# Optimization experiments

Hardware: AMD Instinct MI355X
Metric: run time of the kernel (lower is better)

The kernel has to match this reference:

```python
import jax, jax.numpy as jnp
import numpy as np
from jax import lax

U = 64          # LSTM units (hard-coded in Actor)
EPS = 1e-12     # tf.contrib layer_norm default epsilon


def _ln(x, g, b):
    # layer norm over last axis; g,b broadcast
    mu = jnp.mean(x, axis=-1, keepdims=True)
    var = jnp.mean(jnp.square(x - mu), axis=-1, keepdims=True)
    return (x - mu) * jax.lax.rsqrt(var + EPS) * g + b


def _lstm_layer(xs, W, gamma, beta, gc, bc):
    # xs: (B, T, D); W: (D+U, 4U); gamma,beta: (4, U); gc,bc: (U,)
    B = xs.shape[0]
    c0 = jnp.zeros((B, U), xs.dtype)
    h0 = jnp.zeros((B, U), xs.dtype)

    def step(carry, x_t):
        c, h = carry
        z = jnp.concatenate([x_t, h], axis=-1) @ W          # (B, 4U), no bias
        z = _ln(z.reshape(B, 4, U), gamma, beta)            # per-gate layer norm
        i, j, f, o = z[:, 0], z[:, 1], z[:, 2], z[:, 3]
        new_c = c * jax.nn.sigmoid(f + 1.0) + jax.nn.sigmoid(i) * jnp.tanh(j)
        new_h = jnp.tanh(_ln(new_c, gc, bc)) * jax.nn.sigmoid(o)
        return (new_c, new_h), new_h

    _, hs = lax.scan(step, (c0, h0), jnp.swapaxes(xs, 0, 1))  # hs: (T, B, U)
    return jnp.swapaxes(hs, 0, 1)                             # (B, T, U)


def setup_inputs() -> dict:
    key = jax.random.key(0)
    ks = jax.random.split(key, 8)
    B, T, D, A = 256, 1024, 128, 16
    s1 = 1.0 / np.sqrt(D + U)
    s2 = 1.0 / np.sqrt(U + U)
    return {
        "obss": jax.random.normal(ks[0], (B, T, D), jnp.float32),
        "W1": jax.random.uniform(ks[1], (D + U, 4 * U), jnp.float32, -s1, s1),
        "gamma1": jnp.ones((4, U), jnp.float32),
        "beta1": jnp.zeros((4, U), jnp.float32),
        "gc1": jnp.ones((U,), jnp.float32),
        "bc1": jnp.zeros((U,), jnp.float32),
        "W2": jax.random.uniform(ks[2], (U + U, 4 * U), jnp.float32, -s2, s2),
        "gamma2": jnp.ones((4, U), jnp.float32),
        "beta2": jnp.zeros((4, U), jnp.float32),
        "gc2": jnp.ones((U,), jnp.float32),
        "bc2": jnp.zeros((U,), jnp.float32),
        "Wd": jax.random.uniform(ks[3], (U, A), jnp.float32, -0.003, 0.003),
        "bd": jnp.zeros((A,), jnp.float32),
    }


def reference(obss, W1, gamma1, beta1, gc1, bc1, W2, gamma2, beta2, gc2, bc2, Wd, bd):
    h1 = _lstm_layer(obss, W1, gamma1, beta1, gc1, bc1)   # (B, T, U)
    h2 = _lstm_layer(h1, W2, gamma2, beta2, gc2, bc2)     # (B, T, U)
    return jnp.tanh(h2 @ Wd + bd)                          # (B, T, nb_actions)
```

## Files before the change

### kernel.cpp

```cpp
#include <hip/hip_runtime.h>
#include <math.h>

#define TT 1024
#define DD 128
#define UU 64

__device__ __forceinline__ float sigm(float x) {
    return __builtin_amdgcn_rcpf(1.0f + __expf(-x));
}
__device__ __forceinline__ float tanhfast(float x) {
    float e = __expf(2.0f * x);
    return fmaf(-2.0f, __builtin_amdgcn_rcpf(e + 1.0f), 1.0f);
}

template<int CTRL>
__device__ __forceinline__ float dpp_add(float v) {
    return v + __int_as_float(__builtin_amdgcn_update_dpp(
        0, __float_as_int(v), CTRL, 0xf, 0xf, true));
}
__device__ __forceinline__ float wave_red_sum(float v) {
    v = dpp_add<0x111>(v);
    v = dpp_add<0x112>(v);
    v = dpp_add<0x114>(v);
    v = dpp_add<0x118>(v);
    v = dpp_add<0x142>(v);
    v = dpp_add<0x143>(v);
    return __int_as_float(__builtin_amdgcn_readlane(__float_as_int(v), 63));
}

#define DOT64(res, vptr, WARR) do {                                \
    const float4* _v4 = (const float4*)(vptr);                     \
    float _a0 = 0.f, _a1 = 0.f, _a2 = 0.f, _a3 = 0.f;              \
    _Pragma("unroll")                                              \
    for (int _k = 0; _k < UU / 4; ++_k) {                          \
        float4 _hv = _v4[_k];                                      \
        _a0 = fmaf(_hv.x, WARR[4 * _k + 0], _a0);                  \
        _a1 = fmaf(_hv.y, WARR[4 * _k + 1], _a1);                  \
        _a2 = fmaf(_hv.z, WARR[4 * _k + 2], _a2);                  \
        _a3 = fmaf(_hv.w, WARR[4 * _k + 3], _a3);                  \
    }                                                              \
    res = (_a0 + _a1) + (_a2 + _a3);                               \
} while (0)

__global__ __launch_bounds__(256, 1)
void xgemm(const float* __restrict__ obss, const float* __restrict__ W1,
           float* __restrict__ z1x, int t0, int chsh)
{
    const int tid = threadIdx.x;
    const int CH = 1 << chsh;
    __shared__ __align__(16) float xs[64 * DD];

    const int rbase = blockIdx.x * 64;
    for (int i = tid; i < 64 * (DD / 4); i += 256) {
        int rr = i >> 5;
        int k4 = i & 31;
        int r  = rbase + rr;
        int b  = r >> chsh;
        int tl = r & (CH - 1);
        ((float4*)xs)[rr * 32 + k4] =
            ((const float4*)(obss + ((size_t)b * TT + t0 + tl) * DD))[k4];
    }

    float w[DD];
    #pragma unroll
    for (int k = 0; k < DD; ++k) w[k] = W1[k * 256 + tid];
    __syncthreads();

    for (int rr = 0; rr < 64; rr += 2) {
        float a0=0,a1=0,a2=0,a3=0, b0=0,b1=0,b2=0,b3=0;
        const float4* x0 = (const float4*)(xs + rr * DD);
        const float4* x1 = (const float4*)(xs + (rr + 1) * DD);
        #pragma unroll
        for (int k4 = 0; k4 < DD / 4; ++k4) {
            float4 xv = x0[k4], yv = x1[k4];
            a0 = fmaf(xv.x, w[4*k4+0], a0);
            a1 = fmaf(xv.y, w[4*k4+1], a1);
            a2 = fmaf(xv.z, w[4*k4+2], a2);
            a3 = fmaf(xv.w, w[4*k4+3], a3);
            b0 = fmaf(yv.x, w[4*k4+0], b0);
            b1 = fmaf(yv.y, w[4*k4+1], b1);
            b2 = fmaf(yv.z, w[4*k4+2], b2);
            b3 = fmaf(yv.w, w[4*k4+3], b3);
        }
        size_t r = (size_t)rbase + rr;
        z1x[r * 256 + tid]       = (a0 + a1) + (a2 + a3);
        z1x[(r + 1) * 256 + tid] = (b0 + b1) + (b2 + b3);
    }
}

__global__ __launch_bounds__(512) __attribute__((amdgpu_waves_per_eu(2, 2)))
void lstm_rec(const float* __restrict__ z1x,
              const float* __restrict__ W1, const float* __restrict__ W2,
              const float* __restrict__ gamma1, const float* __restrict__ beta1,
              const float* __restrict__ gc1, const float* __restrict__ bc1,
              const float* __restrict__ gamma2, const float* __restrict__ beta2,
              const float* __restrict__ gc2, const float* __restrict__ bc2,
              const float* __restrict__ Wd, const float* __restrict__ bd,
              float* __restrict__ out, float* __restrict__ state,
              int t0, int nsteps)
{
    const int tid  = threadIdx.x;
    const int b    = blockIdx.x;
    const int gid  = tid >> 8;
    const int stid = tid & 255;
    const int lane = stid & 63;
    const int wav  = stid >> 6;

    __shared__ __align__(16) float zsA[256], zsB[256], z2xs[256];
    __shared__ __align__(16) float h1p[4][UU], h2p[4][UU];
    __shared__ __align__(16) float h2hist[16 * 65];
    __shared__ __align__(16) float wds[UU * 16];
    __shared__ float bds[16];

    float* st = state + (size_t)b * 256;

    if (gid == 0) {
        float w1h[UU], w2x[UU];
        #pragma unroll
        for (int k = 0; k < UU; ++k) w1h[k] = W1[(DD + k) * 256 + stid];
        #pragma unroll
        for (int k = 0; k < UU; ++k) w2x[k] = W2[k * 256 + stid];
        const float g1 = gamma1[stid], bb1 = beta1[stid];
        const float gcl = gc1[lane],  bcl = bc1[lane];
        for (int i = stid; i < UU * 16; i += 256) wds[i] = Wd[i];
        if (stid < 16) bds[stid] = bd[stid];

        float c1, h1v = 0.f;
        if (t0 == 0) { c1 = 0.f; h1p[wav][lane] = 0.f; }
        else         { c1 = st[lane]; h1v = st[64 + lane]; h1p[wav][lane] = h1v; }

        const float* zrow = z1x + (size_t)b * nsteps * 256;
        float zx = zrow[stid];
        __syncthreads();

        #pragma unroll 1
        for (int n = 0; n <= nsteps; ++n) {
            float zxn = zx;
            if (n < nsteps) {
                int tnl = (n + 1 < nsteps) ? n + 1 : n;
                zxn = zrow[(size_t)tnl * 256 + stid];

                float zdot;
                DOT64(zdot, h1p[wav], w1h);
                float z = zx + zdot;
                float s = wave_red_sum(z);
                float q = wave_red_sum(z * z);
                float mu  = s * (1.f/64.f);
                float var = q * (1.f/64.f) - mu * mu;
                float zn  = (z - mu) * __builtin_amdgcn_rsqf(var + 1e-12f) * g1 + bb1;
                zsA[stid] = (wav == 1) ? tanhfast(zn)
                          : (wav == 2) ? sigm(zn + 1.f)
                          :              sigm(zn);
            }
            if ((n & 15) == 1 && n >= 17) {
                int t2p  = n - 2;
                int rloc = stid >> 4;
                int a    = stid & 15;
                float o = bds[a];
                #pragma unroll
                for (int k = 0; k < UU; ++k)
                    o = fmaf(h2hist[rloc * 65 + k], wds[k * 16 + a], o);
                int r = t0 + t2p - 15 + rloc;
                out[((size_t)b * TT + r) * 16 + a] = tanhfast(o);
            }
            __syncthreads();
            if (n < nsteps) {
                float ai = zsA[lane],       aj = zsA[64 + lane];
                float af = zsA[128 + lane], ao = zsA[192 + lane];
                c1 = c1 * af + ai * aj;
                float cs = wave_red_sum(c1);
                float cq = wave_red_sum(c1 * c1);
                float cmu  = cs * (1.f/64.f);
                float cvar = cq * (1.f/64.f) - cmu * cmu;
                float cn   = (c1 - cmu) * __builtin_amdgcn_rsqf(cvar + 1e-12f) * gcl + bcl;
                h1v = tanhfast(cn) * ao;
                h1p[wav][lane] = h1v;
                float zxdot;
                DOT64(zxdot, h1p[wav], w2x);
                z2xs[stid] = zxdot;
            }
            __syncthreads();
            zx = zxn;
        }
        {
            int rloc = stid >> 4;
            int a    = stid & 15;
            float o = bds[a];
            #pragma unroll
            for (int k = 0; k < UU; ++k)
                o = fmaf(h2hist[rloc * 65 + k], wds[k * 16 + a], o);
            int r = t0 + nsteps - 16 + rloc;
            out[((size_t)b * TT + r) * 16 + a] = tanhfast(o);
        }
        if (t0 + nsteps < TT && wav == 0) {
            st[lane]      = c1;
            st[64 + lane] = h1v;
        }
    } else {
        float w2h[UU];
        #pragma unroll
        for (int k = 0; k < UU; ++k) w2h[k] = W2[(UU + k) * 256 + stid];
        const float g2 = gamma2[stid], bb2 = beta2[stid];
        const float gcl = gc2[lane],  bcl = bc2[lane];

        float c2, h2v = 0.f;
        if (t0 == 0) { c2 = 0.f; h2p[wav][lane] = 0.f; }
        else         { c2 = st[128 + lane]; h2v = st[192 + lane]; h2p[wav][lane] = h2v; }
        float z2h = 0.f;
        if (t0 != 0) { DOT64(z2h, h2p[wav], w2h); }
        __syncthreads();

        #pragma unroll 1
        for (int n = 0; n <= nsteps; ++n) {
            if (n >= 1) {
                float z2 = z2xs[stid] + z2h;
                float s2 = wave_red_sum(z2);
                float q2 = wave_red_sum(z2 * z2);
                float mu2  = s2 * (1.f/64.f);
                float var2 = q2 * (1.f/64.f) - mu2 * mu2;
                float zn2  = (z2 - mu2) * __builtin_amdgcn_rsqf(var2 + 1e-12f) * g2 + bb2;
                zsB[stid] = (wav == 1) ? tanhfast(zn2)
                          : (wav == 2) ? sigm(zn2 + 1.f)
                          :              sigm(zn2);
            }
            __syncthreads();
            if (n >= 1) {
                float ai = zsB[lane],       aj = zsB[64 + lane];
                float af = zsB[128 + lane], ao = zsB[192 + lane];
                c2 = c2 * af + ai * aj;
                float cs = wave_red_sum(c2);
                float cq = wave_red_sum(c2 * c2);
                float cmu  = cs * (1.f/64.f);
                float cvar = cq * (1.f/64.f) - cmu * cmu;
                float cn   = (c2 - cmu) * __builtin_amdgcn_rsqf(cvar + 1e-12f) * gcl + bcl;
                h2v = tanhfast(cn) * ao;
                h2p[wav][lane] = h2v;
                if (wav == 0) h2hist[((n - 1) & 15) * 65 + lane] = h2v;
                DOT64(z2h, h2p[wav], w2h);
            }
            __syncthreads();
        }
        if (t0 + nsteps < TT && wav == 0) {
            st[128 + lane] = c2;
            st[192 + lane] = h2v;
        }
    }
}

extern "C" void kernel_launch(void* const* d_in, const int* in_sizes, int n_in,
                              void* d_out, int out_size, void* d_ws, size_t ws_size,
                              hipStream_t stream) {
    (void)in_sizes; (void)n_in; (void)out_size;
    const float* obss   = (const float*)d_in[0];
    const float* W1     = (const float*)d_in[1];
    const float* gamma1 = (const float*)d_in[2];
    const float* beta1  = (const float*)d_in[3];
    const float* gc1    = (const float*)d_in[4];
    const float* bc1    = (const float*)d_in[5];
    const float* W2     = (const float*)d_in[6];
    const float* gamma2 = (const float*)d_in[7];
    const float* beta2  = (const float*)d_in[8];
    const float* gc2    = (const float*)d_in[9];
    const float* bc2    = (const float*)d_in[10];
    const float* Wd     = (const float*)d_in[11];
    const float* bd     = (const float*)d_in[12];
    float* out = (float*)d_out;

    float* state = (float*)d_ws;
    float* z1x   = (float*)((char*)d_ws + (size_t)256 * 256 * sizeof(float));

    int CH = 16;
    for (int c = TT; c >= 16; c >>= 1) {
        size_t need = (size_t)256 * c * 256 * sizeof(float)
                    + (size_t)256 * 256 * sizeof(float);
        if (need <= ws_size) { CH = c; break; }
    }
    int chsh = 31 - __builtin_clz((unsigned)CH);

    for (int t0 = 0; t0 < TT; t0 += CH) {
        xgemm<<<(256 * CH) / 64, 256, 0, stream>>>(obss, W1, z1x, t0, chsh);
        lstm_rec<<<256, 512, 0, stream>>>(z1x, W1, W2,
                                          gamma1, beta1, gc1, bc1,
                                          gamma2, beta2, gc2, bc2,
                                          Wd, bd, out, state, t0, CH);
    }
}
```

Baseline: 1.459 ms.

## Split LSTM recurrence into three wave groups with a deeper layer pipeline

Adds a third 256-thread group that takes over the layer-2 input projection (h1·W2x) and the output dense layer from the layer-1 group. It reads h1 through a two-slot ring buffer, and the layer-2 group's gate/activation step is reordered so the pipeline runs two timesteps deep. The goal is to shorten the per-step critical path of the layer-1 recurrence by moving extra dot products off it. In exchange the block grows to 768 threads at 3 waves per EU, which can cut the register budget per thread, and the loop gains an extra iteration of barriers.

```diff
diff --git a/kernel.cpp b/kernel.cpp
--- a/kernel.cpp
+++ b/kernel.cpp
@@ -88,7 +88,7 @@
     }
 }
 
-__global__ __launch_bounds__(512) __attribute__((amdgpu_waves_per_eu(2, 2)))
+__global__ __launch_bounds__(768) __attribute__((amdgpu_waves_per_eu(3, 3)))
 void lstm_rec(const float* __restrict__ z1x,
               const float* __restrict__ W1, const float* __restrict__ W2,
               const float* __restrict__ gamma1, const float* __restrict__ beta1,
@@ -107,37 +107,35 @@
     const int wav  = stid >> 6;
 
     __shared__ __align__(16) float zsA[256], zsB[256], z2xs[256];
+    __shared__ __align__(16) float h1ring[2][UU];
     __shared__ __align__(16) float h1p[4][UU], h2p[4][UU];
-    __shared__ __align__(16) float h2hist[16 * 65];
+    __shared__ __align__(16) float h2hist[32 * 65];
     __shared__ __align__(16) float wds[UU * 16];
     __shared__ float bds[16];
 
     float* st = state + (size_t)b * 256;
+    const int NS = nsteps;
 
     if (gid == 0) {
-        float w1h[UU], w2x[UU];
+        float w1h[UU];
         #pragma unroll
         for (int k = 0; k < UU; ++k) w1h[k] = W1[(DD + k) * 256 + stid];
-        #pragma unroll
-        for (int k = 0; k < UU; ++k) w2x[k] = W2[k * 256 + stid];
         const float g1 = gamma1[stid], bb1 = beta1[stid];
         const float gcl = gc1[lane],  bcl = bc1[lane];
-        for (int i = stid; i < UU * 16; i += 256) wds[i] = Wd[i];
-        if (stid < 16) bds[stid] = bd[stid];
 
         float c1, h1v = 0.f;
         if (t0 == 0) { c1 = 0.f; h1p[wav][lane] = 0.f; }
         else         { c1 = st[lane]; h1v = st[64 + lane]; h1p[wav][lane] = h1v; }
 
-        const float* zrow = z1x + (size_t)b * nsteps * 256;
+        const float* zrow = z1x + (size_t)b * NS * 256;
         float zx = zrow[stid];
         __syncthreads();
 
         #pragma unroll 1
-        for (int n = 0; n <= nsteps; ++n) {
+        for (int n = 0; n <= NS + 2; ++n) {
             float zxn = zx;
-            if (n < nsteps) {
-                int tnl = (n + 1 < nsteps) ? n + 1 : n;
+            if (n < NS) {
+                int tnl = (n + 1 < NS) ? n + 1 : n;
                 zxn = zrow[(size_t)tnl * 256 + stid];
 
                 float zdot;
@@ -152,19 +150,8 @@
                           : (wav == 2) ? sigm(zn + 1.f)
                           :              sigm(zn);
             }
-            if ((n & 15) == 1 && n >= 17) {
-                int t2p  = n - 2;
-                int rloc = stid >> 4;
-                int a    = stid & 15;
-                float o = bds[a];
-                #pragma unroll
-                for (int k = 0; k < UU; ++k)
-                    o = fmaf(h2hist[rloc * 65 + k], wds[k * 16 + a], o);
-                int r = t0 + t2p - 15 + rloc;
-                out[((size_t)b * TT + r) * 16 + a] = tanhfast(o);
-            }
-            __syncthreads();
-            if (n < nsteps) {
+            __syncthreads();
+            if (n < NS) {
                 float ai = zsA[lane],       aj = zsA[64 + lane];
                 float af = zsA[128 + lane], ao = zsA[192 + lane];
                 c1 = c1 * af + ai * aj;
@@ -175,26 +162,43 @@
                 float cn   = (c1 - cmu) * __builtin_amdgcn_rsqf(cvar + 1e-12f) * gcl + bcl;
                 h1v = tanhfast(cn) * ao;
                 h1p[wav][lane] = h1v;
-                float zxdot;
-                DOT64(zxdot, h1p[wav], w2x);
-                z2xs[stid] = zxdot;
+                if (wav == 0) h1ring[n & 1][lane] = h1v;
             }
             __syncthreads();
             zx = zxn;
         }
-        {
-            int rloc = stid >> 4;
-            int a    = stid & 15;
-            float o = bds[a];
-            #pragma unroll
-            for (int k = 0; k < UU; ++k)
-                o = fmaf(h2hist[rloc * 65 + k], wds[k * 16 + a], o);
-            int r = t0 + nsteps - 16 + rloc;
-            out[((size_t)b * TT + r) * 16 + a] = tanhfast(o);
-        }
-        if (t0 + nsteps < TT && wav == 0) {
+        if (t0 + NS < TT && wav == 0) {
             st[lane]      = c1;
             st[64 + lane] = h1v;
+        }
+    } else if (gid == 1) {
+        float w2x[UU];
+        #pragma unroll
+        for (int k = 0; k < UU; ++k) w2x[k] = W2[k * 256 + stid];
+        for (int i = stid; i < UU * 16; i += 256) wds[i] = Wd[i];
+        if (stid < 16) bds[stid] = bd[stid];
+        __syncthreads();
+
+        #pragma unroll 1
+        for (int n = 0; n <= NS + 2; ++n) {
+            if (n >= 1 && n <= NS) {
+                float zxdot;
+                DOT64(zxdot, h1ring[(n - 1) & 1], w2x);
+                z2xs[stid] = zxdot;
+            }
+            __syncthreads();
+            if ((n & 15) == 2 && n >= 18) {
+                int rloc = stid >> 4;
+                int a    = stid & 15;
+                int m    = n - 18 + rloc;
+                float o = bds[a];
+                const float* hrow = &h2hist[(m & 31) * 65];
+                #pragma unroll
+                for (int k = 0; k < UU; ++k)
+                    o = fmaf(hrow[k], wds[k * 16 + a], o);
+                out[((size_t)b * TT + (t0 + m)) * 16 + a] = tanhfast(o);
+            }
+            __syncthreads();
         }
     } else {
         float w2h[UU];
@@ -211,20 +215,8 @@
         __syncthreads();
 
         #pragma unroll 1
-        for (int n = 0; n <= nsteps; ++n) {
-            if (n >= 1) {
-                float z2 = z2xs[stid] + z2h;
-                float s2 = wave_red_sum(z2);
-                float q2 = wave_red_sum(z2 * z2);
-                float mu2  = s2 * (1.f/64.f);
-                float var2 = q2 * (1.f/64.f) - mu2 * mu2;
-                float zn2  = (z2 - mu2) * __builtin_amdgcn_rsqf(var2 + 1e-12f) * g2 + bb2;
-                zsB[stid] = (wav == 1) ? tanhfast(zn2)
-                          : (wav == 2) ? sigm(zn2 + 1.f)
-                          :              sigm(zn2);
-            }
-            __syncthreads();
-            if (n >= 1) {
+        for (int n = 0; n <= NS + 2; ++n) {
+            if (n >= 2 && n <= NS + 1) {
                 float ai = zsB[lane],       aj = zsB[64 + lane];
                 float af = zsB[128 + lane], ao = zsB[192 + lane];
                 c2 = c2 * af + ai * aj;
@@ -235,12 +227,24 @@
                 float cn   = (c2 - cmu) * __builtin_amdgcn_rsqf(cvar + 1e-12f) * gcl + bcl;
                 h2v = tanhfast(cn) * ao;
                 h2p[wav][lane] = h2v;
-                if (wav == 0) h2hist[((n - 1) & 15) * 65 + lane] = h2v;
+                if (wav == 0) h2hist[((n - 2) & 31) * 65 + lane] = h2v;
                 DOT64(z2h, h2p[wav], w2h);
             }
             __syncthreads();
-        }
-        if (t0 + nsteps < TT && wav == 0) {
+            if (n >= 1 && n <= NS) {
+                float z2 = z2xs[stid] + z2h;
+                float s2 = wave_red_sum(z2);
+                float q2 = wave_red_sum(z2 * z2);
+                float mu2  = s2 * (1.f/64.f);
+                float var2 = q2 * (1.f/64.f) - mu2 * mu2;
+                float zn2  = (z2 - mu2) * __builtin_amdgcn_rsqf(var2 + 1e-12f) * g2 + bb2;
+                zsB[stid] = (wav == 1) ? tanhfast(zn2)
+                          : (wav == 2) ? sigm(zn2 + 1.f)
+                          :              sigm(zn2);
+            }
+            __syncthreads();
+        }
+        if (t0 + NS < TT && wav == 0) {
             st[128 + lane] = c2;
             st[192 + lane] = h2v;
         }
@@ -279,7 +283,7 @@
 
     for (int t0 = 0; t0 < TT; t0 += CH) {
         xgemm<<<(256 * CH) / 64, 256, 0, stream>>>(obss, W1, z1x, t0, chsh);
-        lstm_rec<<<256, 512, 0, stream>>>(z1x, W1, W2,
+        lstm_rec<<<256, 768, 0, stream>>>(z1x, W1, W2,
                                           gamma1, beta1, gc1, bc1,
                                           gamma2, beta2, gc2, bc2,
                                           Wd, bd, out, state, t0, CH);
```

Measured after the change: 1.348 ms. -7.6%, faster.
